# Optimization experiments

Measured on AMD Instinct MI355X. Metric: run time of the kernel, lower is better.

## Reference

```python
import jax, jax.numpy as jnp
import numpy as np

B, T, D = 2, 2048, 1024
N_HEADS, N_KV_HEADS = 16, 4
D_HEAD = D // N_HEADS            # 64
N_GROUPS = N_HEADS // N_KV_HEADS  # 4
ROPE_THETA = 10000.0


def _rope_freqs(t, d_head, theta):
    inv = 1.0 / (theta ** (jnp.arange(0, d_head, 2, dtype=jnp.float32) / d_head))  # (d_head/2,)
    ang = jnp.arange(t, dtype=jnp.float32)[:, None] * inv[None, :]                 # (T, d_head/2)
    return jnp.stack([jnp.cos(ang), jnp.sin(ang)], axis=-1)                        # (T, d_head/2, 2)


def _apply_rope(x, freqs):
    # x: (B, T, H, d_head); freqs: (T, d_head/2, 2) = (cos, sin)
    xr = x.reshape(*x.shape[:-1], -1, 2)          # (B,T,H,d/2,2)
    xre, xim = xr[..., 0], xr[..., 1]
    fre = freqs[None, :, None, :, 0]              # (1,T,1,d/2)
    fim = freqs[None, :, None, :, 1]
    outre = xre * fre - xim * fim
    outim = xre * fim + xim * fre
    return jnp.stack([outre, outim], axis=-1).reshape(x.shape)


def setup_inputs() -> dict:
    key = jax.random.key(0)
    ks = jax.random.split(key, 5)
    x = jax.random.normal(ks[0], (B, T, D), dtype=jnp.float32)
    w_q = jax.random.normal(ks[1], (N_HEADS * D_HEAD, D), dtype=jnp.float32) * 0.02
    w_k = jax.random.normal(ks[2], (N_KV_HEADS * D_HEAD, D), dtype=jnp.float32) * 0.02
    w_v = jax.random.normal(ks[3], (N_KV_HEADS * D_HEAD, D), dtype=jnp.float32) * 0.02
    w_o = jax.random.normal(ks[4], (D, N_HEADS * D_HEAD), dtype=jnp.float32) * 0.02
    rope_freqs = _rope_freqs(T, D_HEAD, ROPE_THETA)
    causal = jnp.tril(jnp.ones((T, T), dtype=bool))
    mask = jnp.where(causal, 0.0, -1e9).astype(jnp.float32)[None, None]  # (1,1,T,T)
    return {"x": x, "rope_freqs": rope_freqs, "mask": mask,
            "w_q": w_q, "w_k": w_k, "w_v": w_v, "w_o": w_o}


def reference(x, rope_freqs, mask, w_q, w_k, w_v, w_o):
    # projections (torch Linear: y = x @ W.T)
    q = jnp.einsum('btd,od->bto', x, w_q).reshape(B, T, N_HEADS, D_HEAD)
    k = jnp.einsum('btd,od->bto', x, w_k).reshape(B, T, N_KV_HEADS, D_HEAD)
    v = jnp.einsum('btd,od->bto', x, w_v).reshape(B, T, N_KV_HEADS, D_HEAD)
    q = _apply_rope(q, rope_freqs)
    k = _apply_rope(k, rope_freqs)
    # GQA: expand KV heads (kv head h -> N_GROUPS contiguous query heads)
    k = jnp.repeat(k, N_GROUPS, axis=2)   # (B,T,H,d)
    v = jnp.repeat(v, N_GROUPS, axis=2)
    q = q.transpose(0, 2, 1, 3)           # (B,H,T,d)
    k = k.transpose(0, 2, 1, 3)
    v = v.transpose(0, 2, 1, 3)
    scale = 1.0 / np.sqrt(D_HEAD).astype(np.float32)
    scores = jnp.einsum('bhqd,bhkd->bhqk', q, k) * scale + mask
    attn = jax.nn.softmax(scores, axis=-1)
    out = jnp.einsum('bhqk,bhkd->bhqd', attn, v)
    out = out.transpose(0, 2, 1, 3).reshape(B, T, N_HEADS * D_HEAD)
    return jnp.einsum('bto,do->btd', out, w_o)
```

## Files before the change

kernel.cpp:

```cpp
#include <hip/hip_runtime.h>
#include <hip/hip_bf16.h>
#include <cstddef>

#define TT   2048
#define NH   16
#define NKV  4
#define DH   64

typedef __bf16 bf16x8 __attribute__((ext_vector_type(8)));
typedef float  f32x4  __attribute__((ext_vector_type(4)));

#define GLD_LDS16(gp, lp)                                                   \
    __builtin_amdgcn_global_load_lds(                                       \
        (const __attribute__((address_space(1))) void*)(gp),                \
        (__attribute__((address_space(3))) void*)(lp), 16, 0, 0)

#if __has_builtin(__builtin_amdgcn_exp2f)
#define EXP2F(x) __builtin_amdgcn_exp2f(x)
#else
#define EXP2F(x) __expf((x) * 0.69314718056f)
#endif

#define QSCALE 0.180336880f

__global__ __launch_bounds__(256)
void cast_kernel(const float* __restrict__ x,  const float* __restrict__ wq,
                 const float* __restrict__ wk, const float* __restrict__ wv,
                 const float* __restrict__ wo,
                 __bf16* __restrict__ xb, __bf16* __restrict__ wqkv,
                 __bf16* __restrict__ wob)
{
    const int g = blockIdx.x * 256 + threadIdx.x;
    const float* src;
    __bf16* dst;
    int off;
    if (g < 1048576)       { src = x;  dst = xb;   off = g; }
    else if (g < 1310720)  { src = wq; dst = wqkv; off = g - 1048576; }
    else if (g < 1376256)  { src = wk; dst = wqkv + 1048576; off = g - 1310720; }
    else if (g < 1441792)  { src = wv; dst = wqkv + 1310720; off = g - 1376256; }
    else                   { src = wo; dst = wob;  off = g - 1441792; }
    const float4 v = *(const float4*)(src + (size_t)off * 4);
    union { __bf16 h[4]; uint2 u; } o;
    o.h[0] = (__bf16)v.x; o.h[1] = (__bf16)v.y;
    o.h[2] = (__bf16)v.z; o.h[3] = (__bf16)v.w;
    *(uint2*)(dst + (size_t)off * 4) = o.u;
}

template<int MODE>
__global__ __launch_bounds__(128)
void mm_kernel(const __bf16* __restrict__ A,
               const __bf16* __restrict__ W,
               const float* __restrict__ rope,
               void* __restrict__ O0, void* __restrict__ O1,
               void* __restrict__ O2)
{
    constexpr int K = 1024;
    __shared__ __bf16 As[128 * 32];
    __shared__ __bf16 Bs[64 * 32];

    const int tid  = threadIdx.x;
    const int lane = tid & 63;
    const int wv   = tid >> 6;
    const int quad = lane >> 4;
    const int lc   = lane & 15;
    const int gm0  = blockIdx.y * 128;
    const int gn0  = blockIdx.x * 64;

    size_t gaA[4], gaB[2];
    int lsA[4], lsB[2];
#pragma unroll
    for (int j = 0; j < 4; j++) {
        const int p = tid + j * 128;
        const int r = p >> 2, q = (p & 3) ^ ((r >> 1) & 3);
        gaA[j] = (size_t)r * K + q * 8;
        lsA[j] = p * 8;
    }
#pragma unroll
    for (int j = 0; j < 2; j++) {
        const int p = tid + j * 128;
        const int r = p >> 2, q = (p & 3) ^ ((r >> 1) & 3);
        gaB[j] = (size_t)r * K + q * 8;
        lsB[j] = p * 8;
    }
    const __bf16* Ag = A + (size_t)gm0 * K;
    const __bf16* Wg = W + (size_t)gn0 * K;

    auto foff = [&](int row) { return (row * 4 + (quad ^ ((row >> 1) & 3))) * 8; };
    int aoff[4], boff[4];
#pragma unroll
    for (int i = 0; i < 4; i++) {
        aoff[i] = foff(wv * 64 + i * 16 + lc);
        boff[i] = foff(i * 16 + lc);
    }

    f32x4 acc[4][4];
#pragma unroll
    for (int i = 0; i < 4; i++)
#pragma unroll
        for (int j = 0; j < 4; j++) acc[i][j] = (f32x4){0.f, 0.f, 0.f, 0.f};

    for (int kt = 0; kt < K; kt += 32) {
        __syncthreads();
#pragma unroll
        for (int j = 0; j < 4; j++) GLD_LDS16(Ag + gaA[j] + kt, As + lsA[j]);
#pragma unroll
        for (int j = 0; j < 2; j++) GLD_LDS16(Wg + gaB[j] + kt, Bs + lsB[j]);
        __syncthreads();

        bf16x8 af[4], bfr[4];
#pragma unroll
        for (int i = 0; i < 4; i++) af[i]  = *(const bf16x8*)&As[aoff[i]];
#pragma unroll
        for (int j = 0; j < 4; j++) bfr[j] = *(const bf16x8*)&Bs[boff[j]];
#pragma unroll
        for (int i = 0; i < 4; i++)
#pragma unroll
            for (int j = 0; j < 4; j++)
                acc[i][j] = __builtin_amdgcn_mfma_f32_16x16x32_bf16(
                    af[i], bfr[j], acc[i][j], 0, 0, 0);
    }

    if (MODE == 0) {
        __bf16* Qo = (__bf16*)O0;
        __bf16* Ko = (__bf16*)O1;
        __bf16* Vo = (__bf16*)O2;
        const int region = (gn0 < 1024) ? 0 : (gn0 < 1280) ? 1 : 2;
#pragma unroll
        for (int i = 0; i < 4; i++) {
#pragma unroll
            for (int r = 0; r < 4; r++) {
                const int grow = gm0 + wv * 64 + i * 16 + quad * 4 + r;
                const int b = grow >> 11, t = grow & 2047;
                const float* rrow = rope + t * 64;
#pragma unroll
                for (int j = 0; j < 4; j++) {
                    const float v = acc[i][j][r];
                    const float partner = __shfl_xor(v, 1, 64);
                    const int col = gn0 + j * 16 + lc;
                    if (region == 0) {
                        const int h = col >> 6, d = col & 63;
                        const float2 cs = *(const float2*)(rrow + (d >> 1) * 2);
                        const float out = v * cs.x + partner * ((d & 1) ? cs.y : -cs.y);
                        Qo[((size_t)(b * NH + h) * TT + t) * DH + d] = (__bf16)(out * QSCALE);
                    } else if (region == 1) {
                        const int ck = col - 1024;
                        const int kh = ck >> 6, d = ck & 63;
                        const float2 cs = *(const float2*)(rrow + (d >> 1) * 2);
                        const float out = v * cs.x + partner * ((d & 1) ? cs.y : -cs.y);
                        Ko[((size_t)(b * NKV + kh) * TT + t) * DH + d] = (__bf16)out;
                    } else {
                        const int cv = col - 1280;
                        const int kh = cv >> 6, d = cv & 63;
                        Vo[((size_t)(b * NKV + kh) * DH + d) * TT + t] = (__bf16)v;
                    }
                }
            }
        }
    } else {
        float* Of = (float*)O0;
#pragma unroll
        for (int i = 0; i < 4; i++)
#pragma unroll
            for (int r = 0; r < 4; r++) {
                const int grow = gm0 + wv * 64 + i * 16 + quad * 4 + r;
#pragma unroll
                for (int j = 0; j < 4; j++)
                    Of[(size_t)grow * 1024 + gn0 + j * 16 + lc] = acc[i][j][r];
            }
    }
}

__global__ __launch_bounds__(128, 2)
void attn_kernel(const __bf16* __restrict__ Q,
                 const __bf16* __restrict__ K,
                 const __bf16* __restrict__ Vt,
                 __bf16* __restrict__ O)
{
    __shared__ __bf16 Ks[64 * 64];
    __shared__ __bf16 Vs[64 * 64];
    __shared__ __bf16 Ps[2][32][72];

    const int tid  = threadIdx.x;
    const int lane = tid & 63;
    const int wv   = tid >> 6;
    const int quad = lane >> 4;
    const int lc   = lane & 15;

    const int a   = blockIdx.x & 31;
    const int rep = blockIdx.x >> 5;
    const int qt  = ((rep >> 3) & 1) ? (31 - a) : a;
    const int b   = rep >> 4;
    const int h   = rep & 15;
    const int kh  = h >> 2;
    const int nk  = qt + 1;

    const __bf16* Kg = K  + (size_t)(b * NKV + kh) * TT * DH;
    const __bf16* Vg = Vt + (size_t)(b * NKV + kh) * DH * TT;

    bf16x8 qb[2][2];
#pragma unroll
    for (int u = 0; u < 2; u++) {
        const __bf16* qp = Q + ((size_t)(b * NH + h) * TT
                                + qt * 64 + wv * 32 + u * 16 + lc) * DH;
        qb[u][0] = *(const bf16x8*)(qp + quad * 8);
        qb[u][1] = *(const bf16x8*)(qp + 32 + quad * 8);
    }

    int koff[4], voff[4], lsl[4];
#pragma unroll
    for (int j = 0; j < 4; j++) {
        const int p  = tid + j * 128;
        const int r  = p >> 3;
        const int qs = (p & 7) ^ (r & 7);
        koff[j] = r * DH + qs * 8;
        voff[j] = r * TT + qs * 8;
        lsl[j]  = p * 8;
    }

    int foff[4][2];
#pragma unroll
    for (int g = 0; g < 4; g++)
#pragma unroll
        for (int c = 0; c < 2; c++)
            foff[g][c] = ((g * 16 + lc) * 8 + ((c * 4 + quad) ^ (lc & 7))) * 8;

    float l_s[2] = {0.f, 0.f};
    f32x4 oacc[2][4];
#pragma unroll
    for (int u = 0; u < 2; u++)
#pragma unroll
        for (int g = 0; g < 4; g++) oacc[u][g] = (f32x4){0.f, 0.f, 0.f, 0.f};

    bf16x8 kr[4], vr[4];
    auto load_regs = [&](int kt) {
        const __bf16* kp = Kg + (size_t)kt * 64 * DH;
        const __bf16* vp = Vg + (size_t)kt * 64;
#pragma unroll
        for (int j = 0; j < 4; j++) {
            kr[j] = *(const bf16x8*)(kp + koff[j]);
            vr[j] = *(const bf16x8*)(vp + voff[j]);
        }
    };
    auto store_lds = [&]() {
#pragma unroll
        for (int j = 0; j < 4; j++) {
            *(bf16x8*)&Ks[lsl[j]] = kr[j];
            *(bf16x8*)&Vs[lsl[j]] = vr[j];
        }
    };

    load_regs(0);
    store_lds();
    if (nk > 1) load_regs(1);
    __syncthreads();

    for (int kt = 0; kt < nk; kt++) {
        bf16x8 ka[4][2];
#pragma unroll
        for (int g = 0; g < 4; g++) {
            ka[g][0] = *(const bf16x8*)&Ks[foff[g][0]];
            ka[g][1] = *(const bf16x8*)&Ks[foff[g][1]];
        }

        const int Dbase = qt * 64 + wv * 32 - kt * 64;

        f32x4 s[2][4];
#pragma unroll
        for (int u = 0; u < 2; u++)
#pragma unroll
            for (int g = 0; g < 4; g++) {
                f32x4 z = (f32x4){0.f, 0.f, 0.f, 0.f};
                z = __builtin_amdgcn_mfma_f32_16x16x32_bf16(ka[g][0], qb[u][0], z, 0, 0, 0);
                z = __builtin_amdgcn_mfma_f32_16x16x32_bf16(ka[g][1], qb[u][1], z, 0, 0, 0);
                s[u][g] = z;
            }

#pragma unroll
        for (int u = 0; u < 2; u++) {
            const int D = Dbase + u * 16;
            if (D < 63) {
                const int thr = D + lc;
#pragma unroll
                for (int g = 0; g < 4; g++)
#pragma unroll
                    for (int r = 0; r < 4; r++)
                        if (g * 16 + quad * 4 + r > thr) s[u][g][r] = -1e30f;
            }
        }

#pragma unroll
        for (int u = 0; u < 2; u++) {
            float rs = 0.f;
#pragma unroll
            for (int g = 0; g < 4; g++) {
#pragma unroll
                for (int r = 0; r < 4; r++) {
                    s[u][g][r] = EXP2F(s[u][g][r]);
                    rs += s[u][g][r];
                }
                union { __bf16 hh[4]; uint2 uu; } pk;
                pk.hh[0] = (__bf16)s[u][g][0]; pk.hh[1] = (__bf16)s[u][g][1];
                pk.hh[2] = (__bf16)s[u][g][2]; pk.hh[3] = (__bf16)s[u][g][3];
                *(uint2*)&Ps[wv][u * 16 + lc][g * 16 + quad * 4] = pk.uu;
            }
            l_s[u] += rs;
        }

        bf16x8 va[4][2];
#pragma unroll
        for (int g = 0; g < 4; g++) {
            va[g][0] = *(const bf16x8*)&Vs[foff[g][0]];
            va[g][1] = *(const bf16x8*)&Vs[foff[g][1]];
        }

#pragma unroll
        for (int u = 0; u < 2; u++) {
            const bf16x8 pb0 = *(const bf16x8*)&Ps[wv][u * 16 + lc][quad * 8];
            const bf16x8 pb1 = *(const bf16x8*)&Ps[wv][u * 16 + lc][32 + quad * 8];
#pragma unroll
            for (int g = 0; g < 4; g++) {
                oacc[u][g] = __builtin_amdgcn_mfma_f32_16x16x32_bf16(va[g][0], pb0, oacc[u][g], 0, 0, 0);
                oacc[u][g] = __builtin_amdgcn_mfma_f32_16x16x32_bf16(va[g][1], pb1, oacc[u][g], 0, 0, 0);
            }
        }

        if (kt + 1 < nk) {
            __syncthreads();
            store_lds();
            if (kt + 2 < nk) load_regs(kt + 2);
            __syncthreads();
        }
    }

#pragma unroll
    for (int u = 0; u < 2; u++) {
        float l = l_s[u];
        l += __shfl_xor(l, 16, 64);
        l += __shfl_xor(l, 32, 64);
        const float inv = 1.f / l;
        const int t = qt * 64 + wv * 32 + u * 16 + lc;
        __bf16* op = O + (size_t)(b * TT + t) * (NH * DH) + h * DH;
#pragma unroll
        for (int g = 0; g < 4; g++) {
            union { __bf16 hh[4]; uint2 uu; } pk;
            pk.hh[0] = (__bf16)(oacc[u][g][0] * inv);
            pk.hh[1] = (__bf16)(oacc[u][g][1] * inv);
            pk.hh[2] = (__bf16)(oacc[u][g][2] * inv);
            pk.hh[3] = (__bf16)(oacc[u][g][3] * inv);
            *(uint2*)(op + g * 16 + quad * 4) = pk.uu;
        }
    }
}

extern "C" void kernel_launch(void* const* d_in, const int* in_sizes, int n_in,
                              void* d_out, int out_size, void* d_ws, size_t ws_size,
                              hipStream_t stream)
{
    const float* x    = (const float*)d_in[0];
    const float* rope = (const float*)d_in[1];
    const float* w_q  = (const float*)d_in[3];
    const float* w_k  = (const float*)d_in[4];
    const float* w_v  = (const float*)d_in[5];
    const float* w_o  = (const float*)d_in[6];
    float* out = (float*)d_out;

    char* ws = (char*)d_ws;
    __bf16* Qb   = (__bf16*)(ws);
    __bf16* Kb   = (__bf16*)(ws + (8  << 20));
    __bf16* Vtb  = (__bf16*)(ws + (10 << 20));
    __bf16* AOb  = (__bf16*)(ws + (12 << 20));
    __bf16* xb   = (__bf16*)(ws + (20 << 20));
    __bf16* Wqkv = (__bf16*)(ws + (28 << 20));
    __bf16* Wob  = (__bf16*)(ws + (31 << 20));

    cast_kernel<<<6656, dim3(256), 0, stream>>>(x, w_q, w_k, w_v, w_o,
                                                xb, Wqkv, Wob);

    dim3 g1(24, 32);
    mm_kernel<0><<<g1, dim3(128), 0, stream>>>(xb, Wqkv, rope,
                                               (void*)Qb, (void*)Kb, (void*)Vtb);

    attn_kernel<<<1024, dim3(128), 0, stream>>>(Qb, Kb, Vtb, AOb);

    dim3 g3(16, 32);
    mm_kernel<1><<<g3, dim3(128), 0, stream>>>(AOb, Wob, rope,
                                               (void*)out, nullptr, nullptr);
}
```

Baseline: 197.1 us.

## Register-prefetch GEMM tiles and transpose block tile to 64x128

The projection GEMM kernel replaces direct global-to-LDS async loads with a register-staged software pipeline that prefetches the tile two K-steps ahead while computing the current one. The block tile changes from 128x64 to 64x128, so the two waves now split the N dimension instead of M. Grids and epilogue indexing are updated to match, and launch bounds request two blocks per CU. The aim is to hide global memory latency behind MFMA work. The cost is extra registers and a VGPR round-trip through LDS stores instead of the direct load path.

```diff
diff --git a/kernel.cpp b/kernel.cpp
--- a/kernel.cpp
+++ b/kernel.cpp
@@ -9,11 +9,6 @@
 
 typedef __bf16 bf16x8 __attribute__((ext_vector_type(8)));
 typedef float  f32x4  __attribute__((ext_vector_type(4)));
-
-#define GLD_LDS16(gp, lp)                                                   \
-    __builtin_amdgcn_global_load_lds(                                       \
-        (const __attribute__((address_space(1))) void*)(gp),                \
-        (__attribute__((address_space(3))) void*)(lp), 16, 0, 0)
 
 #if __has_builtin(__builtin_amdgcn_exp2f)
 #define EXP2F(x) __builtin_amdgcn_exp2f(x)
@@ -47,36 +42,38 @@
 }
 
 template<int MODE>
-__global__ __launch_bounds__(128)
+__global__ __launch_bounds__(128, 2)
 void mm_kernel(const __bf16* __restrict__ A,
                const __bf16* __restrict__ W,
                const float* __restrict__ rope,
                void* __restrict__ O0, void* __restrict__ O1,
                void* __restrict__ O2)
 {
-    constexpr int K = 1024;
-    __shared__ __bf16 As[128 * 32];
-    __shared__ __bf16 Bs[64 * 32];
+    constexpr int K  = 1024;
+    constexpr int NK = K / 32;
+    __shared__ __bf16 As[64 * 32];
+    __shared__ __bf16 Bs[128 * 32];
 
     const int tid  = threadIdx.x;
     const int lane = tid & 63;
     const int wv   = tid >> 6;
     const int quad = lane >> 4;
     const int lc   = lane & 15;
-    const int gm0  = blockIdx.y * 128;
-    const int gn0  = blockIdx.x * 64;
-
-    size_t gaA[4], gaB[2];
-    int lsA[4], lsB[2];
-#pragma unroll
-    for (int j = 0; j < 4; j++) {
+    const int gm0  = blockIdx.y * 64;
+    const int gn0  = blockIdx.x * 128;
+    const int wc0  = wv * 64;
+
+    size_t gaA[2], gaB[4];
+    int lsA[2], lsB[4];
+#pragma unroll
+    for (int j = 0; j < 2; j++) {
         const int p = tid + j * 128;
         const int r = p >> 2, q = (p & 3) ^ ((r >> 1) & 3);
         gaA[j] = (size_t)r * K + q * 8;
         lsA[j] = p * 8;
     }
 #pragma unroll
-    for (int j = 0; j < 2; j++) {
+    for (int j = 0; j < 4; j++) {
         const int p = tid + j * 128;
         const int r = p >> 2, q = (p & 3) ^ ((r >> 1) & 3);
         gaB[j] = (size_t)r * K + q * 8;
@@ -89,8 +86,8 @@
     int aoff[4], boff[4];
 #pragma unroll
     for (int i = 0; i < 4; i++) {
-        aoff[i] = foff(wv * 64 + i * 16 + lc);
-        boff[i] = foff(i * 16 + lc);
+        aoff[i] = foff(i * 16 + lc);
+        boff[i] = foff(wc0 + i * 16 + lc);
     }
 
     f32x4 acc[4][4];
@@ -99,14 +96,27 @@
 #pragma unroll
         for (int j = 0; j < 4; j++) acc[i][j] = (f32x4){0.f, 0.f, 0.f, 0.f};
 
-    for (int kt = 0; kt < K; kt += 32) {
-        __syncthreads();
-#pragma unroll
-        for (int j = 0; j < 4; j++) GLD_LDS16(Ag + gaA[j] + kt, As + lsA[j]);
-#pragma unroll
-        for (int j = 0; j < 2; j++) GLD_LDS16(Wg + gaB[j] + kt, Bs + lsB[j]);
-        __syncthreads();
-
+    bf16x8 ar[2], br[4];
+    auto load_regs = [&](int kt) {
+        const int kb = kt * 32;
+#pragma unroll
+        for (int j = 0; j < 2; j++) ar[j] = *(const bf16x8*)(Ag + gaA[j] + kb);
+#pragma unroll
+        for (int j = 0; j < 4; j++) br[j] = *(const bf16x8*)(Wg + gaB[j] + kb);
+    };
+    auto store_lds = [&]() {
+#pragma unroll
+        for (int j = 0; j < 2; j++) *(bf16x8*)&As[lsA[j]] = ar[j];
+#pragma unroll
+        for (int j = 0; j < 4; j++) *(bf16x8*)&Bs[lsB[j]] = br[j];
+    };
+
+    load_regs(0);
+    store_lds();
+    load_regs(1);
+    __syncthreads();
+
+    for (int kt = 0; kt < NK; kt++) {
         bf16x8 af[4], bfr[4];
 #pragma unroll
         for (int i = 0; i < 4; i++) af[i]  = *(const bf16x8*)&As[aoff[i]];
@@ -118,6 +128,13 @@
             for (int j = 0; j < 4; j++)
                 acc[i][j] = __builtin_amdgcn_mfma_f32_16x16x32_bf16(
                     af[i], bfr[j], acc[i][j], 0, 0, 0);
+
+        if (kt + 1 < NK) {
+            __syncthreads();
+            store_lds();
+            if (kt + 2 < NK) load_regs(kt + 2);
+            __syncthreads();
+        }
     }
 
     if (MODE == 0) {
@@ -129,14 +146,14 @@
         for (int i = 0; i < 4; i++) {
 #pragma unroll
             for (int r = 0; r < 4; r++) {
-                const int grow = gm0 + wv * 64 + i * 16 + quad * 4 + r;
+                const int grow = gm0 + i * 16 + quad * 4 + r;
                 const int b = grow >> 11, t = grow & 2047;
                 const float* rrow = rope + t * 64;
 #pragma unroll
                 for (int j = 0; j < 4; j++) {
                     const float v = acc[i][j][r];
                     const float partner = __shfl_xor(v, 1, 64);
-                    const int col = gn0 + j * 16 + lc;
+                    const int col = gn0 + wc0 + j * 16 + lc;
                     if (region == 0) {
                         const int h = col >> 6, d = col & 63;
                         const float2 cs = *(const float2*)(rrow + (d >> 1) * 2);
@@ -162,10 +179,10 @@
         for (int i = 0; i < 4; i++)
 #pragma unroll
             for (int r = 0; r < 4; r++) {
-                const int grow = gm0 + wv * 64 + i * 16 + quad * 4 + r;
+                const int grow = gm0 + i * 16 + quad * 4 + r;
 #pragma unroll
                 for (int j = 0; j < 4; j++)
-                    Of[(size_t)grow * 1024 + gn0 + j * 16 + lc] = acc[i][j][r];
+                    Of[(size_t)grow * 1024 + gn0 + wc0 + j * 16 + lc] = acc[i][j][r];
             }
     }
 }
@@ -376,13 +393,13 @@
     cast_kernel<<<6656, dim3(256), 0, stream>>>(x, w_q, w_k, w_v, w_o,
                                                 xb, Wqkv, Wob);
 
-    dim3 g1(24, 32);
+    dim3 g1(12, 64);
     mm_kernel<0><<<g1, dim3(128), 0, stream>>>(xb, Wqkv, rope,
                                                (void*)Qb, (void*)Kb, (void*)Vtb);
 
     attn_kernel<<<1024, dim3(128), 0, stream>>>(Qb, Kb, Vtb, AOb);
 
-    dim3 g3(16, 32);
+    dim3 g3(8, 64);
     mm_kernel<1><<<g3, dim3(128), 0, stream>>>(AOb, Wob, rope,
                                                (void*)out, nullptr, nullptr);
 }
```

Result: faster. 186.7 us (-5.3%).
